# Kernel tuning notes

Measured on AMD Instinct MI355X. Metric: run time of the kernel, lower is better.

## Reference

```python
import jax, jax.numpy as jnp
import numpy as np

D_MODEL = 1024
N_HEADS = 16
HEAD_DIM = D_MODEL // N_HEADS


def setup_inputs() -> dict:
    key = jax.random.key(0)
    k_x, k_qkv, k_out = jax.random.split(key, 3)
    B, T = 4, 2048
    x = jax.random.normal(k_x, (B, T, D_MODEL), dtype=jnp.float32)
    # Linear(bias=False): y = x @ W, with W stored as [in, out]
    W_qkv = jax.random.normal(k_qkv, (D_MODEL, 3 * D_MODEL), dtype=jnp.float32) * (D_MODEL ** -0.5)
    W_out = jax.random.normal(k_out, (D_MODEL, D_MODEL), dtype=jnp.float32) * (D_MODEL ** -0.5)
    return {"x": x, "W_qkv": W_qkv, "W_out": W_out}


def reference(x, W_qkv, W_out):
    B, T, C = x.shape
    H, Dh = N_HEADS, HEAD_DIM
    scale = 1.0 / jnp.sqrt(jnp.asarray(Dh, dtype=x.dtype))

    qkv = x @ W_qkv  # [B,T,3C]
    q, k, v = jnp.split(qkv, 3, axis=-1)

    def split_heads(t):
        return t.reshape(B, T, H, Dh).transpose(0, 2, 1, 3)  # [B,H,T,Dh]

    q, k, v = split_heads(q), split_heads(k), split_heads(v)

    scores = jnp.einsum('bhqd,bhkd->bhqk', q, k) * scale  # [B,H,T,T]
    causal = jnp.tril(jnp.ones((T, T), dtype=bool))
    scores = jnp.where(causal, scores, jnp.asarray(-jnp.inf, dtype=scores.dtype))
    attn = jax.nn.softmax(scores, axis=-1)
    # dropout p=0.0 -> identity
    out = jnp.einsum('bhqk,bhkd->bhqd', attn, v)  # [B,H,T,Dh]
    out = out.transpose(0, 2, 1, 3).reshape(B, T, C)
    return out @ W_out
```

## Files before the change

kernel.cpp:

```cpp
#include <hip/hip_runtime.h>
#include <stdint.h>

typedef unsigned short u16;
typedef float f32x4 __attribute__((ext_vector_type(4)));
typedef short s16x8 __attribute__((ext_vector_type(8)));

#define SEQ 2048
#define DM 1024
#define NH 16
#define HD 64
#define BATCH 4
#define ROWS (BATCH*SEQ)
#define QTILES (SEQ/64)

__device__ __forceinline__ u16 f32_bf16(float f) {
  union { float f; uint32_t u; } c; c.f = f;
  uint32_t u = c.u;
  return (u16)((u + 0x7fffu + ((u >> 16) & 1u)) >> 16);
}
__device__ __forceinline__ u16 f32_bf16_trunc(float f) {
  union { float f; uint32_t u; } c; c.f = f;
  return (u16)(c.u >> 16);
}

#define GLOAD_LDS16(g, l) __builtin_amdgcn_global_load_lds( \
    (__attribute__((address_space(1))) void*)(g),           \
    (__attribute__((address_space(3))) void*)(l), 16, 0, 0)

__global__ __launch_bounds__(256) void cast_bf16_k(const float* __restrict__ in,
                                                   u16* __restrict__ out, int n4) {
  int i = blockIdx.x * 256 + threadIdx.x;
  if (i >= n4) return;
  float4 v = ((const float4*)in)[i];
  ushort4 o;
  o.x = f32_bf16(v.x); o.y = f32_bf16(v.y); o.z = f32_bf16(v.z); o.w = f32_bf16(v.w);
  ((ushort4*)out)[i] = o;
}

__global__ __launch_bounds__(256) void cast_transpose_k(const float* __restrict__ in,
                                                        u16* __restrict__ out, int R, int C) {
  __shared__ float tile[32][33];
  int c0 = blockIdx.x * 32, r0 = blockIdx.y * 32;
  int t = threadIdx.x;
  int lr = t >> 3, lc = (t & 7) * 4;
  float4 v = *(const float4*)(in + (size_t)(r0 + lr) * C + c0 + lc);
  tile[lr][lc] = v.x; tile[lr][lc + 1] = v.y; tile[lr][lc + 2] = v.z; tile[lr][lc + 3] = v.w;
  __syncthreads();
  ushort4 o;
  o.x = f32_bf16(tile[lc + 0][lr]);
  o.y = f32_bf16(tile[lc + 1][lr]);
  o.z = f32_bf16(tile[lc + 2][lr]);
  o.w = f32_bf16(tile[lc + 3][lr]);
  *(ushort4*)(out + (size_t)(c0 + lr) * R + r0 + lc) = o;
}

#define QSCALE 0.18033688011112042f

template<int EPI>
__global__ __launch_bounds__(256) void gemm_bt(
    const u16* __restrict__ A, const u16* __restrict__ Bt,
    float* __restrict__ Cf, u16* __restrict__ Qo, u16* __restrict__ Ko, u16* __restrict__ Vo,
    int M, int N, int K)
{
  __shared__ u16 As[128 * 32];
  __shared__ u16 Bs[128 * 32];
  int t = threadIdx.x;
  int m0 = blockIdx.y * 128, n0 = blockIdx.x * 128;

  int srow = t >> 2, scol8 = (t & 3) * 8;
  const u16* Ag0 = A  + (size_t)(m0 + srow) * K + scol8;
  const u16* Ag1 = A  + (size_t)(m0 + 64 + srow) * K + scol8;
  const u16* Bg0 = Bt + (size_t)(n0 + srow) * K + scol8;
  const u16* Bg1 = Bt + (size_t)(n0 + 64 + srow) * K + scol8;
  u16* Al0 = As + t * 8;  u16* Al1 = As + 2048 + t * 8;
  u16* Bl0 = Bs + t * 8;  u16* Bl1 = Bs + 2048 + t * 8;

  int lane = t & 63, w = t >> 6;
  int m16 = lane & 15, quad = lane >> 4;
  int wr = (w >> 1) * 64, wc = (w & 1) * 64;

  f32x4 acc[4][4];
#pragma unroll
  for (int mi = 0; mi < 4; ++mi)
#pragma unroll
    for (int ni = 0; ni < 4; ++ni)
#pragma unroll
      for (int r = 0; r < 4; ++r) acc[mi][ni][r] = 0.f;

  for (int k0 = 0; k0 < K; k0 += 32) {
    __syncthreads();
    GLOAD_LDS16(Ag0 + k0, Al0);
    GLOAD_LDS16(Ag1 + k0, Al1);
    GLOAD_LDS16(Bg0 + k0, Bl0);
    GLOAD_LDS16(Bg1 + k0, Bl1);
    __syncthreads();
    s16x8 af[4], bf[4];
#pragma unroll
    for (int mi = 0; mi < 4; ++mi)
      af[mi] = *(const s16x8*)(As + (wr + mi * 16 + m16) * 32 + quad * 8);
#pragma unroll
    for (int ni = 0; ni < 4; ++ni)
      bf[ni] = *(const s16x8*)(Bs + (wc + ni * 16 + m16) * 32 + quad * 8);
#pragma unroll
    for (int mi = 0; mi < 4; ++mi)
#pragma unroll
      for (int ni = 0; ni < 4; ++ni)
        acc[mi][ni] = __builtin_amdgcn_mfma_f32_16x16x32_bf16(af[mi], bf[ni], acc[mi][ni], 0, 0, 0);
  }

  if (EPI == 0) {
#pragma unroll
    for (int mi = 0; mi < 4; ++mi) {
      int gr = m0 + wr + mi * 16 + quad * 4;
#pragma unroll
      for (int ni = 0; ni < 4; ++ni) {
        int gc = n0 + wc + ni * 16 + m16;
#pragma unroll
        for (int r = 0; r < 4; ++r)
          Cf[(size_t)(gr + r) * N + gc] = acc[mi][ni][r];
      }
    }
  } else {
#pragma unroll
    for (int mi = 0; mi < 4; ++mi) {
      int gr = m0 + wr + mi * 16 + quad * 4;
      int b = gr >> 11, tt = gr & 2047;
#pragma unroll
      for (int ni = 0; ni < 4; ++ni) {
        int gc = n0 + wc + ni * 16 + m16;
        int sec = gc >> 10, rem = gc & 1023, h = rem >> 6, d = rem & 63;
        if (sec == 0) {
#pragma unroll
          for (int r = 0; r < 4; ++r)
            Qo[(((size_t)b * NH + h) * SEQ + tt + r) * HD + d] = f32_bf16(acc[mi][ni][r] * QSCALE);
        } else if (sec == 1) {
#pragma unroll
          for (int r = 0; r < 4; ++r)
            Ko[(((size_t)b * NH + h) * SEQ + tt + r) * HD + d] = f32_bf16(acc[mi][ni][r]);
        } else {
          ushort4 o;
          o.x = f32_bf16(acc[mi][ni][0]); o.y = f32_bf16(acc[mi][ni][1]);
          o.z = f32_bf16(acc[mi][ni][2]); o.w = f32_bf16(acc[mi][ni][3]);
          *(ushort4*)&Vo[(((size_t)b * NH + h) * HD + d) * SEQ + tt] = o;
        }
      }
    }
  }
}

__global__ __launch_bounds__(256) void attn_k(
    const u16* __restrict__ Q, const u16* __restrict__ K,
    const u16* __restrict__ Vt_g,
    u16* __restrict__ O)
{
  __shared__ u16 Ks[64][72];
  __shared__ u16 Vt[64][72];
  __shared__ u16 Ps[4][16][72];
  int bh = blockIdx.y;
  int t = threadIdx.x, w = t >> 6, lane = t & 63;
  int m16 = lane & 15, quad = lane >> 4;
  int b = bh >> 4, h = bh & 15;

  int srow = t >> 2, sc = (t & 3) * 16;
  const u16* Kg0 = K    + ((size_t)bh * SEQ + srow) * HD  + sc;
  const u16* Vg0 = Vt_g + ((size_t)bh * HD  + srow) * SEQ + sc;

  for (int half = 0; half < 2; ++half) {
    int qt = half ? (QTILES - 1 - (int)blockIdx.x) : (int)blockIdx.x;
    int q0 = qt * 64;

    const u16* Qb = Q + ((size_t)bh * SEQ + q0 + w * 16 + m16) * HD + quad * 8;
    s16x8 qf0 = *(const s16x8*)Qb;
    s16x8 qf1 = *(const s16x8*)(Qb + 32);

    f32x4 acco[4];
    float l_part[4];
#pragma unroll
    for (int r = 0; r < 4; ++r) l_part[r] = 0.f;
#pragma unroll
    for (int ni = 0; ni < 4; ++ni)
#pragma unroll
      for (int r = 0; r < 4; ++r) acco[ni][r] = 0.f;

    for (int kt = 0; kt <= qt; ++kt) {
      uint4 kv0 = *(const uint4*)(Kg0 + (size_t)kt * 64 * HD);
      uint4 kv1 = *(const uint4*)(Kg0 + (size_t)kt * 64 * HD + 8);
      uint4 vv0 = *(const uint4*)(Vg0 + kt * 64);
      uint4 vv1 = *(const uint4*)(Vg0 + kt * 64 + 8);
      __syncthreads();
      *(uint4*)&Ks[srow][sc]     = kv0;
      *(uint4*)&Ks[srow][sc + 8] = kv1;
      *(uint4*)&Vt[srow][sc]     = vv0;
      *(uint4*)&Vt[srow][sc + 8] = vv1;
      __syncthreads();

      f32x4 sacc[4];
#pragma unroll
      for (int ni = 0; ni < 4; ++ni)
#pragma unroll
        for (int r = 0; r < 4; ++r) sacc[ni][r] = 0.f;
#pragma unroll
      for (int ni = 0; ni < 4; ++ni) {
        s16x8 kf0 = *(const s16x8*)&Ks[ni * 16 + m16][quad * 8];
        s16x8 kf1 = *(const s16x8*)&Ks[ni * 16 + m16][32 + quad * 8];
        sacc[ni] = __builtin_amdgcn_mfma_f32_16x16x32_bf16(qf0, kf0, sacc[ni], 0, 0, 0);
        sacc[ni] = __builtin_amdgcn_mfma_f32_16x16x32_bf16(qf1, kf1, sacc[ni], 0, 0, 0);
      }
      if (kt == qt) {
#pragma unroll
        for (int ni = 0; ni < 4; ++ni)
#pragma unroll
          for (int r = 0; r < 4; ++r)
            if (ni * 16 + m16 > w * 16 + quad * 4 + r) sacc[ni][r] = -1e30f;
      }

#pragma unroll
      for (int ni = 0; ni < 4; ++ni)
#pragma unroll
        for (int r = 0; r < 4; ++r) {
          float p = __builtin_amdgcn_exp2f(sacc[ni][r]);
          l_part[r] += p;
          Ps[w][quad * 4 + r][ni * 16 + m16] = f32_bf16_trunc(p);
        }

#pragma unroll
      for (int ks = 0; ks < 2; ++ks) {
        s16x8 pf = *(const s16x8*)&Ps[w][m16][ks * 32 + quad * 8];
#pragma unroll
        for (int ni = 0; ni < 4; ++ni) {
          s16x8 vf = *(const s16x8*)&Vt[ni * 16 + m16][ks * 32 + quad * 8];
          acco[ni] = __builtin_amdgcn_mfma_f32_16x16x32_bf16(pf, vf, acco[ni], 0, 0, 0);
        }
      }
    }

    float l[4];
#pragma unroll
    for (int r = 0; r < 4; ++r) l[r] = l_part[r];
#pragma unroll
    for (int off = 1; off < 16; off <<= 1)
#pragma unroll
      for (int r = 0; r < 4; ++r) l[r] += __shfl_xor(l[r], off, 64);

#pragma unroll
    for (int r = 0; r < 4; ++r) {
      float inv = 1.f / l[r];
      int trow = q0 + w * 16 + quad * 4 + r;
      size_t base = ((size_t)(b * SEQ + trow)) * DM + h * HD;
#pragma unroll
      for (int ni = 0; ni < 4; ++ni)
        O[base + ni * 16 + m16] = f32_bf16(acco[ni][r] * inv);
    }
  }
}

extern "C" void kernel_launch(void* const* d_in, const int* in_sizes, int n_in,
                              void* d_out, int out_size, void* d_ws, size_t ws_size,
                              hipStream_t stream) {
  const float* x    = (const float*)d_in[0];
  const float* Wqkv = (const float*)d_in[1];
  const float* Wout = (const float*)d_in[2];
  float* out = (float*)d_out;

  u16* ws = (u16*)d_ws;
  size_t off = 0;
  u16* x_bf   = ws + off; off += (size_t)ROWS * DM;
  u16* wqkv_t = ws + off; off += (size_t)(3 * DM) * DM;
  u16* wout_t = ws + off; off += (size_t)DM * DM;
  u16* Qb     = ws + off; off += (size_t)BATCH * NH * SEQ * HD;
  u16* Kb     = ws + off; off += (size_t)BATCH * NH * SEQ * HD;
  u16* Vb     = ws + off; off += (size_t)BATCH * NH * SEQ * HD;
  u16* AO     = ws + off; off += (size_t)ROWS * DM;

  cast_bf16_k<<<(ROWS * DM / 4 + 255) / 256, 256, 0, stream>>>(x, x_bf, ROWS * DM / 4);
  cast_transpose_k<<<dim3(3 * DM / 32, DM / 32), 256, 0, stream>>>(Wqkv, wqkv_t, DM, 3 * DM);
  cast_transpose_k<<<dim3(DM / 32, DM / 32), 256, 0, stream>>>(Wout, wout_t, DM, DM);
  gemm_bt<1><<<dim3(3 * DM / 128, ROWS / 128), 256, 0, stream>>>(
      x_bf, wqkv_t, nullptr, Qb, Kb, Vb, ROWS, 3 * DM, DM);
  attn_k<<<dim3(QTILES / 2, BATCH * NH), 256, 0, stream>>>(Qb, Kb, Vb, AO);
  gemm_bt<0><<<dim3(DM / 128, ROWS / 128), 256, 0, stream>>>(
      AO, wout_t, out, nullptr, nullptr, nullptr, ROWS, DM, DM);
}
```

Before: 284.1 us.

## Replace QKV projection GEMM with 256x256 four-stage pipelined MFMA kernel

```diff
diff --git a/kernel.cpp b/kernel.cpp
--- a/kernel.cpp
+++ b/kernel.cpp
@@ -56,6 +56,141 @@
 
 #define QSCALE 0.18033688011112042f
 
+
+__device__ __forceinline__ f32x4 mfma16(s16x8 a, s16x8 b, f32x4 c) {
+  return __builtin_amdgcn_mfma_f32_16x16x32_bf16(a, b, c, 0, 0, 0);
+}
+
+template<int STG, int ENDVM>
+__device__ __forceinline__ void tile_body(
+    const u16* lAc, const u16* lBc, u16* lAs, u16* lBs,
+    const u16* gA0, const u16* gA1, const u16* gB0, const u16* gB1,
+    int d0, int d1, int aoff, int boff, f32x4 (&acc)[8][4])
+{
+  s16x8 af[4], bfr[4];
+#pragma unroll
+  for (int ni = 0; ni < 4; ++ni) bfr[ni] = *(const s16x8*)&lBc[boff + ni * 512];
+#pragma unroll
+  for (int mi = 0; mi < 4; ++mi) af[mi] = *(const s16x8*)&lAc[aoff + mi * 512];
+  if (STG) { GLOAD_LDS16(gA0, lAs + d0); GLOAD_LDS16(gA1, lAs + d1); }
+  __builtin_amdgcn_s_barrier();
+  asm volatile("s_waitcnt lgkmcnt(0)" ::: "memory");
+  __builtin_amdgcn_sched_barrier(0);
+  __builtin_amdgcn_s_setprio(1);
+#pragma unroll
+  for (int mi = 0; mi < 4; ++mi)
+#pragma unroll
+    for (int ni = 0; ni < 4; ++ni)
+      acc[mi][ni] = mfma16(af[mi], bfr[ni], acc[mi][ni]);
+  __builtin_amdgcn_s_setprio(0);
+  __builtin_amdgcn_sched_barrier(0);
+  __builtin_amdgcn_s_barrier();
+#pragma unroll
+  for (int mi = 0; mi < 4; ++mi) af[mi] = *(const s16x8*)&lAc[aoff + 2048 + mi * 512];
+  if (STG) { GLOAD_LDS16(gB0, lBs + d0); GLOAD_LDS16(gB1, lBs + d1); }
+  __builtin_amdgcn_s_barrier();
+  asm volatile("s_waitcnt lgkmcnt(0)" ::: "memory");
+  __builtin_amdgcn_sched_barrier(0);
+  __builtin_amdgcn_s_setprio(1);
+#pragma unroll
+  for (int mi = 0; mi < 4; ++mi)
+#pragma unroll
+    for (int ni = 0; ni < 4; ++ni)
+      acc[4 + mi][ni] = mfma16(af[mi], bfr[ni], acc[4 + mi][ni]);
+  __builtin_amdgcn_s_setprio(0);
+  __builtin_amdgcn_sched_barrier(0);
+  if (ENDVM == 8)      asm volatile("s_waitcnt vmcnt(8)" ::: "memory");
+  else if (ENDVM == 4) asm volatile("s_waitcnt vmcnt(4)" ::: "memory");
+  else if (ENDVM == 0) asm volatile("s_waitcnt vmcnt(0)" ::: "memory");
+  __builtin_amdgcn_s_barrier();
+  __builtin_amdgcn_sched_barrier(0);
+}
+
+__global__ __launch_bounds__(512, 2) void qkv_gemm(
+    const u16* __restrict__ A, const u16* __restrict__ Bt,
+    u16* __restrict__ Qo, u16* __restrict__ Ko, u16* __restrict__ Vo)
+{
+  __shared__ u16 lA[4][8192];
+  __shared__ u16 lB[4][8192];
+  int t = threadIdx.x;
+
+  int flat = blockIdx.y * 12 + blockIdx.x;
+  int swz = (flat & 7) * 48 + (flat >> 3);
+  int by = swz / 12, bx = swz - by * 12;
+  int m0 = by * 256, n0 = bx * 256;
+
+  int lane = t & 63, w = t >> 6;
+  int m16 = lane & 15, quad = lane >> 4;
+  int wm = w >> 2, wn = w & 3;
+
+  int r0 = t >> 2;
+  int scol = ((t & 3) ^ ((t >> 3) & 3)) * 8;
+  const u16* Ag0 = A  + (size_t)(m0 + r0) * DM + scol;
+  const u16* Ag1 = A  + (size_t)(m0 + 128 + r0) * DM + scol;
+  const u16* Bg0 = Bt + (size_t)(n0 + r0) * DM + scol;
+  const u16* Bg1 = Bt + (size_t)(n0 + 128 + r0) * DM + scol;
+  int d0 = t * 8, d1 = 4096 + t * 8;
+
+  int ka = (quad ^ ((m16 >> 1) & 3)) * 8;
+  int aoff = (wm * 128 + m16) * 32 + ka;
+  int boff = (wn * 64 + m16) * 32 + ka;
+
+  f32x4 acc[8][4];
+#pragma unroll
+  for (int mi = 0; mi < 8; ++mi)
+#pragma unroll
+    for (int ni = 0; ni < 4; ++ni)
+#pragma unroll
+      for (int r = 0; r < 4; ++r) acc[mi][ni][r] = 0.f;
+
+#pragma unroll
+  for (int kt = 0; kt < 3; ++kt) {
+    GLOAD_LDS16(Ag0 + kt * 32, lA[kt] + d0);
+    GLOAD_LDS16(Ag1 + kt * 32, lA[kt] + d1);
+    GLOAD_LDS16(Bg0 + kt * 32, lB[kt] + d0);
+    GLOAD_LDS16(Bg1 + kt * 32, lB[kt] + d1);
+  }
+  asm volatile("s_waitcnt vmcnt(8)" ::: "memory");
+  __builtin_amdgcn_s_barrier();
+  __builtin_amdgcn_sched_barrier(0);
+
+  for (int T = 0; T <= 28; ++T) {
+    int cur = T & 3, stg = (T + 3) & 3;
+    tile_body<1, 8>(lA[cur], lB[cur], lA[stg], lB[stg],
+                    Ag0 + (T + 3) * 32, Ag1 + (T + 3) * 32,
+                    Bg0 + (T + 3) * 32, Bg1 + (T + 3) * 32,
+                    d0, d1, aoff, boff, acc);
+  }
+  tile_body<0, 4>(lA[1], lB[1], lA[0], lB[0], Ag0, Ag1, Bg0, Bg1, d0, d1, aoff, boff, acc);
+  tile_body<0, 0>(lA[2], lB[2], lA[0], lB[0], Ag0, Ag1, Bg0, Bg1, d0, d1, aoff, boff, acc);
+  tile_body<0, -1>(lA[3], lB[3], lA[0], lB[0], Ag0, Ag1, Bg0, Bg1, d0, d1, aoff, boff, acc);
+
+#pragma unroll
+  for (int mi = 0; mi < 8; ++mi) {
+    int gr = m0 + wm * 128 + mi * 16 + quad * 4;
+    int b = gr >> 11, tt = gr & 2047;
+#pragma unroll
+    for (int ni = 0; ni < 4; ++ni) {
+      int gc = n0 + wn * 64 + ni * 16 + m16;
+      int sec = gc >> 10, rem = gc & 1023, h = rem >> 6, d = rem & 63;
+      if (sec == 0) {
+#pragma unroll
+        for (int r = 0; r < 4; ++r)
+          Qo[(((size_t)b * NH + h) * SEQ + tt + r) * HD + d] = f32_bf16(acc[mi][ni][r] * QSCALE);
+      } else if (sec == 1) {
+#pragma unroll
+        for (int r = 0; r < 4; ++r)
+          Ko[(((size_t)b * NH + h) * SEQ + tt + r) * HD + d] = f32_bf16(acc[mi][ni][r]);
+      } else {
+        ushort4 o;
+        o.x = f32_bf16(acc[mi][ni][0]); o.y = f32_bf16(acc[mi][ni][1]);
+        o.z = f32_bf16(acc[mi][ni][2]); o.w = f32_bf16(acc[mi][ni][3]);
+        *(ushort4*)&Vo[(((size_t)b * NH + h) * HD + d) * SEQ + tt] = o;
+      }
+    }
+  }
+}
+
 template<int EPI>
 __global__ __launch_bounds__(256) void gemm_bt(
     const u16* __restrict__ A, const u16* __restrict__ Bt,
@@ -275,8 +410,7 @@
   cast_bf16_k<<<(ROWS * DM / 4 + 255) / 256, 256, 0, stream>>>(x, x_bf, ROWS * DM / 4);
   cast_transpose_k<<<dim3(3 * DM / 32, DM / 32), 256, 0, stream>>>(Wqkv, wqkv_t, DM, 3 * DM);
   cast_transpose_k<<<dim3(DM / 32, DM / 32), 256, 0, stream>>>(Wout, wout_t, DM, DM);
-  gemm_bt<1><<<dim3(3 * DM / 128, ROWS / 128), 256, 0, stream>>>(
-      x_bf, wqkv_t, nullptr, Qb, Kb, Vb, ROWS, 3 * DM, DM);
+  qkv_gemm<<<dim3(12, 32), 512, 0, stream>>>(x_bf, wqkv_t, Qb, Kb, Vb);
   attn_k<<<dim3(QTILES / 2, BATCH * NH), 256, 0, stream>>>(Qb, Kb, Vb, AO);
   gemm_bt<0><<<dim3(DM / 128, ROWS / 128), 256, 0, stream>>>(
       AO, wout_t, out, nullptr, nullptr, nullptr, ROWS, DM, DM);
```

Result: no change. 288.4 us (+1.5%).
